# Performance work log

Hardware: AMD Instinct MI355X
Metric: run time of the kernel (lower is better)

The kernel has to match this reference:

```python
import jax, jax.numpy as jnp
import numpy as np

M, L, P, KK = 8, 3, 12, 9  # n_heads, n_levels, n_points, patch_size**2

def lrelu(v):
    return jnp.where(v >= 0, v, 0.1 * v)

def conv2d(x, w, b, pad):
    y = jax.lax.conv_general_dilated(x, w, (1, 1), [(pad, pad), (pad, pad)], dimension_numbers=('NCHW', 'OIHW', 'NCHW'))
    return y + b[None, :, None, None]

def trunk(x, w1, b1, w2, b2, w3, b3, w4, b4):
    h = lrelu(conv2d(x, w1, b1, 0))
    h = lrelu(conv2d(h, w2, b2, 1))
    h = lrelu(conv2d(h, w3, b3, 1))
    return conv2d(h, w4, b4, 0)

def grid_sample(img, gx, gy, align_corners):
    # img [N,C,H,W]; gx,gy [N,Q] normalized to [-1,1]; bilinear, zeros padding
    N, C, H, W = img.shape
    if align_corners:
        ix = (gx + 1.0) * 0.5 * (W - 1)
        iy = (gy + 1.0) * 0.5 * (H - 1)
    else:
        ix = ((gx + 1.0) * W - 1.0) * 0.5
        iy = ((gy + 1.0) * H - 1.0) * 0.5
    ix0 = jnp.floor(ix); iy0 = jnp.floor(iy)
    wx1 = ix - ix0; wy1 = iy - iy0
    flat = img.reshape(N, C, H * W)
    def gather(xi, yi, wgt):
        valid = (xi >= 0) & (xi <= W - 1) & (yi >= 0) & (yi <= H - 1)
        idx = (jnp.clip(yi, 0, H - 1) * W + jnp.clip(xi, 0, W - 1)).astype(jnp.int32)
        v = jnp.take_along_axis(flat, idx[:, None, :], axis=2)
        return v * (wgt * valid)[:, None, :]
    return (gather(ix0, iy0, (1 - wx1) * (1 - wy1)) + gather(ix0 + 1, iy0, wx1 * (1 - wy1))
            + gather(ix0, iy0 + 1, (1 - wx1) * wy1) + gather(ix0 + 1, iy0 + 1, wx1 * wy1))

def flow_warp(img, flow):
    # img [n,c,h,w]; flow [n,2,h,w] in pixels; torch grid_sample align_corners=True, zeros padding
    n, c, h, w = img.shape
    gy, gx = jnp.meshgrid(jnp.arange(h, dtype=img.dtype), jnp.arange(w, dtype=img.dtype), indexing='ij')
    gxn = 2.0 * (gx[None] + flow[:, 0]) / max(w - 1, 1) - 1.0
    gyn = 2.0 * (gy[None] + flow[:, 1]) / max(h - 1, 1) - 1.0
    return grid_sample(img, gxn.reshape(n, -1), gyn.reshape(n, -1), True).reshape(n, c, h, w)

def msdeform_attn(value, loc, attn, h, w):
    # pytorch MSDeformAttn core: value [N,L*HW,M,D]; loc [N,HW,M,L,Pt,2]; attn [N,HW,M,L,Pt]
    N, _, _, D = value.shape
    HW = h * w
    Pt = loc.shape[4]
    grids = 2.0 * loc - 1.0
    sampled = []
    for l in range(L):
        v = value[:, l * HW:(l + 1) * HW].transpose(0, 2, 3, 1).reshape(N * M, D, h, w)
        g = grids[:, :, :, l].transpose(0, 2, 1, 3, 4).reshape(N * M, HW * Pt, 2)
        s = grid_sample(v, g[..., 0], g[..., 1], False)  # [N*M, D, HW*Pt]
        sampled.append(s.reshape(N * M, D, HW, Pt))
    sampled = jnp.concatenate(sampled, axis=-1)  # [N*M, D, HW, L*Pt]
    aw = attn.transpose(0, 2, 1, 3, 4).reshape(N * M, HW, L * Pt)
    out = jnp.einsum('ndqp,nqp->nqd', sampled, aw)
    return out.reshape(N, M, HW, D).transpose(0, 2, 1, 3).reshape(N, HW, M * D)

def _forward(x, flow_1, flow_2, flip_flow_1, flip_flow_2, aw_w1, aw_b1, aw_w2, aw_b2, aw_w3, aw_b3, aw_w4, aw_b4, so_w1, so_b1, so_w2, so_b2, so_w3, so_b3, so_w4, so_b4, po_w1, po_b1, po_w2, po_b2, po_w3, po_b3, po_w4, po_b4, vp_w, vp_b, op_w1, op_b1, op_w2, op_b2):
    n, t, c, h, w = x.shape
    HW = h * w
    flow_cn1 = flow_1
    flow_cn2 = flow_1 + flow_warp(flow_2, flow_cn1)
    warp1 = flow_warp(x[:, 1], flow_cn1)
    warp2 = flow_warp(x[:, 2], flow_cn2)
    extra = jnp.concatenate([x[:, 0], warp1, warp2, flow_cn1, flow_cn2], axis=1)  # [n, 3c+4, h, w]
    value = conv2d(x.reshape(n, t * c, h, w), vp_w, vp_b, 0)
    off = trunk(extra, so_w1, so_b1, so_w2, so_b2, so_w3, so_b3, so_w4, so_b4)
    aw = trunk(extra, aw_w1, aw_b1, aw_w2, aw_b2, aw_w3, aw_b3, aw_w4, aw_b4)
    po = trunk(extra, po_w1, po_b1, po_w2, po_b2, po_w3, po_b3, po_w4, po_b4)
    value = value.reshape(n, t, c, HW).transpose(0, 1, 3, 2).reshape(n, t * HW, M, c // M)
    off = off.reshape(n, -1, HW).transpose(0, 2, 1).reshape(n, HW, M, L, P, 2)
    po = po.reshape(n, -1, HW).transpose(0, 2, 1).reshape(n, HW, M, L, P)
    po = jax.nn.sigmoid(po) * 3.0
    aw = aw.reshape(n, -1, HW).transpose(0, 2, 1).reshape(n, HW, M, L * P * KK)
    aw = jax.nn.softmax(aw, axis=-1).reshape(n, HW, M, L, P * KK)
    # flow-guided per-level offsets: level0 zeros, level1 flow_cn1, level2 flow_cn2
    f1 = flow_cn1.reshape(n, 2, HW).transpose(0, 2, 1)
    f2 = flow_cn2.reshape(n, 2, HW).transpose(0, 2, 1)
    fstack = jnp.stack([jnp.zeros_like(f1), f1, f2], axis=2)  # [n,HW,L,2]
    off = off + fstack[:, :, None, :, None, :]
    # 3x3 patch around each sampling point, scaled by learned patch offsets
    a = jnp.arange(-1, 2, dtype=x.dtype)
    pnx, pny = jnp.meshgrid(a, a, indexing='ij')
    p_n = jnp.stack([pnx, pny], axis=-1).reshape(KK, 2)
    off = off[..., None, :] + p_n * po[..., None, None]  # [n,HW,M,L,P,KK,2]
    off = off.reshape(n, HW, M, L, P * KK, 2)
    # reference points (valid ratios == 1)
    ry = (jnp.arange(h, dtype=x.dtype) + 0.5) / h
    rx = (jnp.arange(w, dtype=x.dtype) + 0.5) / w
    gy, gx = jnp.meshgrid(ry, rx, indexing='ij')
    ref = jnp.stack([gx, gy], axis=-1).reshape(1, HW, 1, 1, 1, 2)
    norm = jnp.array([w, h], dtype=x.dtype)
    loc = ref + off / norm
    out = msdeform_attn(value, loc, aw, h, w)  # [n, HW, c]
    feat = out.reshape(n, h, w, c).transpose(0, 3, 1, 2)
    res = conv2d(lrelu(conv2d(feat, op_w1, op_b1, 0)), op_w2, op_b2, 0)
    return res + x[:, 0]

def setup_inputs():
    key = jax.random.key(0)
    keys = jax.random.split(key, 64)
    it = iter(range(64))
    def nrm(shape, scale):
        return jax.random.normal(keys[next(it)], shape, jnp.float32) * scale
    n, t, c, h, w = 1, 3, 64, 64, 64
    Cin = t * c + 4  # 196
    d = {}
    d['x'] = nrm((n, t, c, h, w), 1.0)
    for nm in ['flow_1', 'flow_2', 'flip_flow_1', 'flip_flow_2']:
        d[nm] = nrm((n, 2, h, w), 1.5)
    def branch(prefix, out_ch, final_scale):
        d[prefix + '_w1'] = nrm((64, Cin, 1, 1), 1.0 / np.sqrt(Cin))
        d[prefix + '_b1'] = nrm((64,), 0.01)
        d[prefix + '_w2'] = nrm((64, 64, 3, 3), 1.0 / np.sqrt(64 * 9))
        d[prefix + '_b2'] = nrm((64,), 0.01)
        d[prefix + '_w3'] = nrm((64, 64, 3, 3), 1.0 / np.sqrt(64 * 9))
        d[prefix + '_b3'] = nrm((64,), 0.01)
        d[prefix + '_w4'] = nrm((out_ch, 64, 1, 1), final_scale)
        d[prefix + '_b4'] = nrm((out_ch,), 0.01)
    branch('aw', M * L * P * KK, 0.01)
    branch('so', M * L * P * 2, 0.01)
    branch('po', M * L * P, 0.01)
    d['vp_w'] = nrm((t * c, t * c, 1, 1), 1.0 / np.sqrt(t * c))
    d['vp_b'] = nrm((t * c,), 0.01)
    d['op_w1'] = nrm((c, c, 1, 1), 1.0 / np.sqrt(c))
    d['op_b1'] = nrm((c,), 0.01)
    d['op_w2'] = nrm((c, c, 1, 1), 1.0 / np.sqrt(c))
    d['op_b2'] = nrm((c,), 0.01)
    return d

def reference(x, flow_1, flow_2, flip_flow_1, flip_flow_2, aw_w1, aw_b1, aw_w2, aw_b2, aw_w3, aw_b3, aw_w4, aw_b4, so_w1, so_b1, so_w2, so_b2, so_w3, so_b3, so_w4, so_b4, po_w1, po_b1, po_w2, po_b2, po_w3, po_b3, po_w4, po_b4, vp_w, vp_b, op_w1, op_b1, op_w2, op_b2):
    return _forward(x, flow_1, flow_2, flip_flow_1, flip_flow_2, aw_w1, aw_b1, aw_w2, aw_b2, aw_w3, aw_b3, aw_w4, aw_b4, so_w1, so_b1, so_w2, so_b2, so_w3, so_b3, so_w4, so_b4, po_w1, po_b1, po_w2, po_b2, po_w3, po_b3, po_w4, po_b4, vp_w, vp_b, op_w1, op_b1, op_w2, op_b2)
```

## Files before the change

kernel.cpp:

```cpp
#include <hip/hip_runtime.h>
#include <hip/hip_bf16.h>
#include <math.h>

#define HWN 4096
#define VROW 72
#define VYP 36
#define VSZ_B (24 * VYP * VROW * 16)

typedef __attribute__((ext_vector_type(8))) short short8;
typedef __attribute__((ext_vector_type(4))) float f32x4;
typedef __attribute__((ext_vector_type(2))) float f32x2;

__device__ __forceinline__ float lrelu_f(float v) { return v >= 0.f ? v : 0.1f * v; }

__device__ __forceinline__ unsigned short f2bf(float f) {
  union { float f; unsigned u; } v; v.f = f;
  unsigned r = v.u + 0x7fff + ((v.u >> 16) & 1);
  return (unsigned short)(r >> 16);
}
__device__ __forceinline__ float bf2f(unsigned short u) {
  union { unsigned u; float f; } v; v.u = ((unsigned)u) << 16; return v.f;
}
__device__ __forceinline__ float bf_lo(unsigned u) {
  union { unsigned u; float f; } v; v.u = u << 16; return v.f;
}
__device__ __forceinline__ float bf_hi(unsigned u) {
  union { unsigned u; float f; } v; v.u = u & 0xffff0000u; return v.f;
}
template <bool HI>
__device__ __forceinline__ f32x2 cvt8(unsigned u) {
  return __builtin_amdgcn_cvt_pk_f32_fp8((int)u, HI);
}

__device__ __forceinline__ float bilin_zero(const float* __restrict__ img, float ix, float iy) {
  float fx0 = floorf(ix), fy0 = floorf(iy);
  int x0 = (int)fx0, y0 = (int)fy0;
  float wx1 = ix - fx0, wy1 = iy - fy0;
  float wx0 = 1.f - wx1, wy0 = 1.f - wy1;
  float acc = 0.f;
  if ((unsigned)y0 < 64u) {
    if ((unsigned)x0 < 64u)       acc += wx0 * wy0 * img[y0 * 64 + x0];
    if ((unsigned)(x0 + 1) < 64u) acc += wx1 * wy0 * img[y0 * 64 + x0 + 1];
  }
  if ((unsigned)(y0 + 1) < 64u) {
    if ((unsigned)x0 < 64u)       acc += wx0 * wy1 * img[(y0 + 1) * 64 + x0];
    if ((unsigned)(x0 + 1) < 64u) acc += wx1 * wy1 * img[(y0 + 1) * 64 + x0 + 1];
  }
  return acc;
}

__global__ void k_pre(
    const float* __restrict__ x, const float* __restrict__ flow1, const float* __restrict__ flow2,
    const float* so_w4, const float* po_w4, const float* aw_w4,
    const float* so_b4, const float* po_b4, const float* aw_b4,
    const float* so_b1, const float* po_b1, const float* aw_b1,
    const float* so_b2, const float* po_b2, const float* aw_b2,
    const float* so_b3, const float* po_b3, const float* aw_b3,
    const float* so_w1, const float* po_w1, const float* aw_w1,
    const float* so_w2, const float* po_w2, const float* aw_w2,
    const float* so_w3, const float* po_w3, const float* aw_w3,
    const float* op_w1, const float* op_w2, const float* vp_w,
    unsigned short* Wtail, float* btail, float* b1c, float* b2c, float* b3c,
    unsigned short* o1b, unsigned short* o2b, unsigned short* W1,
    unsigned short* W2g, unsigned short* W3g, unsigned short* vpb,
    unsigned short* xb, float* fcn2, unsigned char* v8) {
  __shared__ unsigned short tile[64 * 65];
  __shared__ unsigned short wrow[576];
  int gx = blockIdx.x;
  int tid = threadIdx.x;
  if (gx < 864) {
    int t = gx * 256 + tid;
    int row = t >> 6, k = t & 63;
    float v = row < 576 ? so_w4[row * 64 + k]
            : row < 864 ? po_w4[(row - 576) * 64 + k]
                        : aw_w4[(row - 864) * 64 + k];
    Wtail[t] = f2bf(v);
  } else if (gx < 912) {
    int t = (gx - 864) * 256 + tid;
    if (t < 3456) {
      btail[t] = t < 576 ? so_b4[t] : t < 864 ? po_b4[t - 576] : aw_b4[t - 864];
    } else if (t < 3648) {
      int i = t - 3456; b1c[i] = i < 64 ? so_b1[i] : i < 128 ? po_b1[i - 64] : aw_b1[i - 128];
    } else if (t < 3840) {
      int i = t - 3648; b2c[i] = i < 64 ? so_b2[i] : i < 128 ? po_b2[i - 64] : aw_b2[i - 128];
    } else if (t < 4032) {
      int i = t - 3840; b3c[i] = i < 64 ? so_b3[i] : i < 128 ? po_b3[i - 64] : aw_b3[i - 128];
    } else if (t < 8128) {
      o1b[t - 4032] = f2bf(op_w1[t - 4032]);
    } else if (t < 12224) {
      o2b[t - 8128] = f2bf(op_w2[t - 8128]);
    }
  } else if (gx < 1080) {
    int t = (gx - 912) * 256 + tid;
    if (t < 192 * 224) {
      int row = t / 224, k = t % 224;
      int tr = row >> 6, lco = row & 63;
      const float* s = tr == 0 ? so_w1 : tr == 1 ? po_w1 : aw_w1;
      W1[t] = (k < 196) ? f2bf(s[lco * 196 + k]) : (unsigned short)0;
    }
  } else if (gx < 1464) {
    int b = gx - 1080;
    int which = b >= 192;
    b &= 191;
    int tr = b >> 6, co = b & 63;
    const float* s;
    if (!which) s = tr == 0 ? so_w2 : tr == 1 ? po_w2 : aw_w2;
    else        s = tr == 0 ? so_w3 : tr == 1 ? po_w3 : aw_w3;
    unsigned short* d = which ? W3g : W2g;
#pragma unroll
    for (int j = tid; j < 576; j += 256) wrow[j] = f2bf(s[co * 576 + j]);
    __syncthreads();
#pragma unroll
    for (int j = tid; j < 576; j += 256)
      d[((size_t)tr * 64 + co) * 576 + j] = wrow[(j & 63) * 9 + (j >> 6)];
  } else if (gx < 1608) {
    int t = (gx - 1464) * 256 + tid;
    if (t < 192 * 192) vpb[t] = f2bf(vp_w[t]);
  } else if (gx < 1800) {
    int b = gx - 1608;
    int ptile = b & 63, cg = b >> 6;
    int px = tid & 63, ch0 = (tid >> 6) * 16;
#pragma unroll
    for (int i = 0; i < 16; i++) {
      float v = x[(size_t)(cg * 64 + ch0 + i) * HWN + ptile * 64 + px];
      tile[(ch0 + i) * 65 + px] = f2bf(v);
    }
    __syncthreads();
    int c = tid & 63, pl0 = (tid >> 6) * 16;
#pragma unroll
    for (int i = 0; i < 16; i++)
      xb[(size_t)(ptile * 64 + pl0 + i) * 192 + cg * 64 + c] = tile[c * 65 + pl0 + i];
  } else if (gx < 1816) {
    int p = (gx - 1800) * 256 + tid;
    int px = p & 63, py = p >> 6;
    float fx = flow1[p], fy = flow1[HWN + p];
    float ix = (float)px + fx, iy = (float)py + fy;
    fcn2[p] = fx + bilin_zero(flow2, ix, iy);
    fcn2[HWN + p] = fy + bilin_zero(flow2 + HWN, ix, iy);
  } else {
    int i = (gx - 1816) * 256 + tid;
    if (i < 2 * VSZ_B / 16) ((uint4*)v8)[i] = make_uint4(0, 0, 0, 0);
  }
}

__global__ void k_extra(const unsigned short* __restrict__ xb, const float* __restrict__ flow1,
                        const float* __restrict__ fcn2, unsigned short* __restrict__ extra) {
  int w = threadIdx.x >> 6, c = threadIdx.x & 63;
  int p = blockIdx.x * 4 + w;
  int px = p & 63, py = p >> 6;
  float fx1 = flow1[p], fy1 = flow1[HWN + p];
  float fx2 = fcn2[p],  fy2 = fcn2[HWN + p];
  extra[(size_t)p * 224 + c] = xb[(size_t)p * 192 + c];
#pragma unroll
  for (int lev = 0; lev < 2; lev++) {
    float ix = (float)px + (lev ? fx2 : fx1);
    float iy = (float)py + (lev ? fy2 : fy1);
    float fx0 = floorf(ix), fy0 = floorf(iy);
    int x0 = (int)fx0, y0 = (int)fy0;
    float wx1 = ix - fx0, wy1 = iy - fy0;
    float wx0 = 1.f - wx1, wy0 = 1.f - wy1;
    int coff = (lev + 1) * 64;
    float acc = 0.f;
    if ((unsigned)y0 < 64u) {
      if ((unsigned)x0 < 64u)       acc += wx0 * wy0 * bf2f(xb[(size_t)(y0 * 64 + x0) * 192 + coff + c]);
      if ((unsigned)(x0 + 1) < 64u) acc += wx1 * wy0 * bf2f(xb[(size_t)(y0 * 64 + x0 + 1) * 192 + coff + c]);
    }
    if ((unsigned)(y0 + 1) < 64u) {
      if ((unsigned)x0 < 64u)       acc += wx0 * wy1 * bf2f(xb[(size_t)((y0 + 1) * 64 + x0) * 192 + coff + c]);
      if ((unsigned)(x0 + 1) < 64u) acc += wx1 * wy1 * bf2f(xb[(size_t)((y0 + 1) * 64 + x0 + 1) * 192 + coff + c]);
    }
    extra[(size_t)p * 224 + coff + c] = f2bf(acc);
  }
  if (c < 2) {
    extra[(size_t)p * 224 + 192 + c] = f2bf(flow1[c * HWN + p]);
    extra[(size_t)p * 224 + 194 + c] = f2bf(fcn2[c * HWN + p]);
  }
  if (c < 28) extra[(size_t)p * 224 + 196 + c] = 0;
}

__global__ __launch_bounds__(128) void k_gemm2(
    const unsigned short* __restrict__ A0, const unsigned short* __restrict__ Wm0,
    const float* __restrict__ bias0, unsigned short* __restrict__ out0,
    const unsigned short* __restrict__ A1, const unsigned short* __restrict__ Wm1,
    const float* __restrict__ bias1, unsigned short* __restrict__ out1) {
  int z = blockIdx.z;
  const unsigned short* A = z ? A1 : A0;
  const unsigned short* Wm = z ? Wm1 : Wm0;
  const float* bias = z ? bias1 : bias0;
  unsigned short* out = z ? out1 : out0;
  int K = z ? 224 : 192;

  int wv = threadIdx.x >> 6;
  int l = threadIdx.x & 63;
  int lm = l & 15, lq = l >> 4;
  int p0 = blockIdx.x * 32 + wv * 16;
  int co0 = blockIdx.y * 32;

  f32x4 acc[2];
#pragma unroll
  for (int nt = 0; nt < 2; nt++) {
    float bv = bias[co0 + nt * 16 + lm];
    acc[nt] = (f32x4){bv, bv, bv, bv};
  }
  const unsigned short* ap = A + (size_t)(p0 + lm) * K + lq * 8;
  const unsigned short* wp = Wm + (size_t)(co0 + lm) * K + lq * 8;
  for (int k0 = 0; k0 < K; k0 += 32) {
    short8 af = *(const short8*)(ap + k0);
#pragma unroll
    for (int nt = 0; nt < 2; nt++) {
      short8 bf = *(const short8*)(wp + (size_t)nt * 16 * K + k0);
      acc[nt] = __builtin_amdgcn_mfma_f32_16x16x32_bf16(af, bf, acc[nt], 0, 0, 0);
    }
  }
#pragma unroll
  for (int nt = 0; nt < 2; nt++) {
    int co = co0 + nt * 16 + lm;
#pragma unroll
    for (int r = 0; r < 4; r++) {
      int p = p0 + lq * 4 + r;
      float v = acc[nt][r];
      if (z) v = lrelu_f(v);
      out[(size_t)p * 192 + co] = f2bf(v);
    }
  }
}

__global__ __launch_bounds__(128) void k_conv3g(const unsigned short* __restrict__ h,
                                                const unsigned short* __restrict__ Wm,
                                                const float* __restrict__ bias,
                                                unsigned short* __restrict__ out) {
  int wv = threadIdx.x >> 6;
  int l = threadIdx.x & 63;
  int lm = l & 15, lq = l >> 4;
  int p0 = blockIdx.x * 32 + wv * 16;
  int co0 = blockIdx.y * 16;
  int t = blockIdx.z;
  int p = p0 + lm;
  int px = p & 63, py = p >> 6;

  float bv = bias[t * 64 + co0 + lm];
  f32x4 acc = (f32x4){bv, bv, bv, bv};
  const unsigned short* wp = Wm + ((size_t)t * 64 + co0 + lm) * 576 + lq * 8;
#pragma unroll
  for (int kidx = 0; kidx < 9; kidx++) {
    int ky = kidx / 3, kx = kidx % 3;
    int pp = p + (ky - 1) * 64 + (kx - 1);
    bool valid = ((unsigned)(px + kx - 1) < 64u) && ((unsigned)(py + ky - 1) < 64u);
    const unsigned short* apb = h + (size_t)pp * 192 + t * 64 + lq * 8;
#pragma unroll
    for (int c2 = 0; c2 < 2; c2++) {
      short8 af = {};
      if (valid) af = *(const short8*)(apb + c2 * 32);
      short8 bf = *(const short8*)(wp + kidx * 64 + c2 * 32);
      acc = __builtin_amdgcn_mfma_f32_16x16x32_bf16(af, bf, acc, 0, 0, 0);
    }
  }
#pragma unroll
  for (int r = 0; r < 4; r++) {
    int po_ = p0 + lq * 4 + r;
    out[(size_t)po_ * 192 + t * 64 + co0 + lm] = f2bf(lrelu_f(acc[r]));
  }
}

__global__ __launch_bounds__(256) void k_tail(const unsigned short* __restrict__ A,
                                              const unsigned short* __restrict__ Wm,
                                              const float* __restrict__ bias,
                                              unsigned short* __restrict__ out,
                                              const unsigned short* __restrict__ vsb,
                                              unsigned char* __restrict__ v8) {
  if (blockIdx.y >= 108) {
    int i = ((blockIdx.y - 108) * 64 + blockIdx.x) * 256 + threadIdx.x;
    int lm = i % 24, p = i / 24;
    uint4 vv = ((const uint4*)vsb)[p * 24 + lm];
    int lo = 0, hi = 0;
    lo = __builtin_amdgcn_cvt_pk_fp8_f32(bf_lo(vv.x), bf_hi(vv.x), lo, false);
    lo = __builtin_amdgcn_cvt_pk_fp8_f32(bf_lo(vv.y), bf_hi(vv.y), lo, true);
    hi = __builtin_amdgcn_cvt_pk_fp8_f32(bf_lo(vv.z), bf_hi(vv.z), hi, false);
    hi = __builtin_amdgcn_cvt_pk_fp8_f32(bf_lo(vv.w), bf_hi(vv.w), hi, true);
    uint2 pk; pk.x = (unsigned)lo; pk.y = (unsigned)hi;
    int y = p >> 6, xx = p & 63;
    int ypA = (y >> 1) + 1, slotA = y & 1;
    int ypB = (y + 1) >> 1, slotB = (y & 1) ^ 1;
    *(uint2*)(v8 + (((lm * VYP + ypA) * VROW + xx + 2) * 16 + slotA * 8)) = pk;
    *(uint2*)(v8 + VSZ_B + (((lm * VYP + ypB) * VROW + xx + 2) * 16 + slotB * 8)) = pk;
    return;
  }
  int wv = threadIdx.x >> 6;
  int l = threadIdx.x & 63;
  int lm = l & 15, lq = l >> 4;
  int p0 = blockIdx.x * 64 + wv * 16;
  int co0 = blockIdx.y * 32;
  int t = (co0 < 576) ? 0 : (co0 < 864 ? 1 : 2);

  f32x4 acc[2];
#pragma unroll
  for (int nt = 0; nt < 2; nt++) {
    float bv = bias[co0 + nt * 16 + lm];
    acc[nt] = (f32x4){bv, bv, bv, bv};
  }
  const unsigned short* ap = A + (size_t)(p0 + lm) * 192 + t * 64 + lq * 8;
  const unsigned short* wp = Wm + (size_t)(co0 + lm) * 64 + lq * 8;
#pragma unroll
  for (int k0 = 0; k0 < 64; k0 += 32) {
    short8 af = *(const short8*)(ap + k0);
#pragma unroll
    for (int nt = 0; nt < 2; nt++) {
      short8 bf = *(const short8*)(wp + (size_t)nt * 16 * 64 + k0);
      acc[nt] = __builtin_amdgcn_mfma_f32_16x16x32_bf16(af, bf, acc[nt], 0, 0, 0);
    }
  }
#pragma unroll
  for (int nt = 0; nt < 2; nt++) {
    int co = co0 + nt * 16 + lm;
#pragma unroll
    for (int r = 0; r < 4; r++) {
      int p = p0 + lq * 4 + r;
      float v = acc[nt][r];
      if (t == 2) v = __expf(v);
      else if (t == 1) v = 3.f * __builtin_amdgcn_rcpf(1.f + __expf(-v));
      out[(size_t)p * 3456 + co] = f2bf(v);
    }
  }
}

__global__ __launch_bounds__(256, 4) void k_msdeform(
    const unsigned char* __restrict__ v8,
    const unsigned short* __restrict__ to,
    const float* __restrict__ flow1, const float* __restrict__ fcn2,
    unsigned short* __restrict__ featb) {
  int yl = threadIdx.x & 15;
  int p = blockIdx.x * 16 + (threadIdx.x >> 4);
  int m = blockIdx.y;
  int px = p & 63, py = p >> 6;

  float fx1 = flow1[p], fy1 = flow1[HWN + p];
  float fx2 = fcn2[p],  fy2 = fcn2[HWN + p];

  const unsigned short* row = to + (size_t)p * 3456;

  f32x2 accv[4];
#pragma unroll
  for (int d = 0; d < 4; d++) accv[d] = (f32x2){0.f, 0.f};
  float wsum = 0.f;

#pragma unroll 1
  for (int pair = yl; pair < 36; pair += 16) {
    int lv = pair / 12, pt = pair % 12;
    float fx = (lv == 1) ? fx1 : ((lv == 2) ? fx2 : 0.f);
    float fy = (lv == 1) ? fy1 : ((lv == 2) ? fy2 : 0.f);
    int ch = (m * 3 + lv) * 12 + pt;
    unsigned ow = *(const unsigned*)(row + ch * 2);
    float ox = bf_lo(ow);
    float oy = bf_hi(ow);
    float s = bf2f(row[576 + ch]);
    float bx = (float)px + ox + fx;
    float by = (float)py + oy + fy;
    int lmoff = (lv * 8 + m) * (VYP * VROW * 16);
    const unsigned short* lgp = row + 864 + m * 324 + lv * 108 + pt * 9;
#pragma unroll 3
    for (int kk = 0; kk < 9; kk++) {
      float pnx = (float)(kk / 3 - 1);
      float pny = (float)(kk % 3 - 1);
      float ix = bx + pnx * s;
      float iy = by + pny * s;
      float wgt = bf2f(lgp[kk]);
      wsum += wgt;

      float fx0 = floorf(ix), fy0 = floorf(iy);
      float wx1 = ix - fx0, wy1 = iy - fy0;
      float wx0 = 1.f - wx1, wy0 = 1.f - wy1;
      int x0 = min(max((int)fx0, -2), 66);
      int y0 = min(max((int)fy0, -2), 66);
      int par = y0 & 1;
      int yp = (y0 + 2 - par) >> 1;
      const unsigned char* vb = v8 + par * VSZ_B + lmoff + (yp * VROW + x0 + 2) * 16;

      uint4 qa = *(const uint4*)vb;
      uint4 qb = *(const uint4*)(vb + 16);

      float w00 = wgt * wx0 * wy0, w01 = wgt * wx0 * wy1;
      float w10 = wgt * wx1 * wy0, w11 = wgt * wx1 * wy1;
      f32x2 W00 = (f32x2){w00, w00}, W01 = (f32x2){w01, w01};
      f32x2 W10 = (f32x2){w10, w10}, W11 = (f32x2){w11, w11};

      accv[0] += W00 * cvt8<false>(qa.x) + W01 * cvt8<false>(qa.z)
               + W10 * cvt8<false>(qb.x) + W11 * cvt8<false>(qb.z);
      accv[1] += W00 * cvt8<true>(qa.x)  + W01 * cvt8<true>(qa.z)
               + W10 * cvt8<true>(qb.x)  + W11 * cvt8<true>(qb.z);
      accv[2] += W00 * cvt8<false>(qa.y) + W01 * cvt8<false>(qa.w)
               + W10 * cvt8<false>(qb.y) + W11 * cvt8<false>(qb.w);
      accv[3] += W00 * cvt8<true>(qa.y)  + W01 * cvt8<true>(qa.w)
               + W10 * cvt8<true>(qb.y)  + W11 * cvt8<true>(qb.w);
    }
  }
#pragma unroll
  for (int mask = 1; mask < 16; mask <<= 1) {
    wsum += __shfl_xor(wsum, mask);
#pragma unroll
    for (int d = 0; d < 4; d++) {
      accv[d].x += __shfl_xor(accv[d].x, mask);
      accv[d].y += __shfl_xor(accv[d].y, mask);
    }
  }
  if (yl < 8) {
    float inv = __builtin_amdgcn_rcpf(wsum);
    float r = 0.f;
#pragma unroll
    for (int d = 0; d < 8; d++) {
      float v = (d & 1) ? accv[d >> 1].y : accv[d >> 1].x;
      r = (d == yl) ? v : r;
    }
    featb[(size_t)p * 64 + m * 8 + yl] = f2bf(r * inv);
  }
}

__global__ __launch_bounds__(128) void k_opout(const unsigned short* __restrict__ featb,
                                               const unsigned short* __restrict__ o1b,
                                               const float* __restrict__ bias1,
                                               const unsigned short* __restrict__ o2b,
                                               const float* __restrict__ bias2,
                                               const float* __restrict__ x,
                                               float* __restrict__ out) {
  __shared__ unsigned short hop[32 * 72];
  int wv = threadIdx.x >> 6;
  int l = threadIdx.x & 63;
  int lm = l & 15, lq = l >> 4;
  int bp0 = blockIdx.x * 32;

  f32x4 acc1[4];
#pragma unroll
  for (int nt = 0; nt < 4; nt++) {
    float bv = bias1[nt * 16 + lm];
    acc1[nt] = (f32x4){bv, bv, bv, bv};
  }
  const unsigned short* ap = featb + (size_t)(bp0 + wv * 16 + lm) * 64 + lq * 8;
#pragma unroll
  for (int k0 = 0; k0 < 64; k0 += 32) {
    short8 af = *(const short8*)(ap + k0);
#pragma unroll
    for (int nt = 0; nt < 4; nt++) {
      short8 bf = *(const short8*)(o1b + (size_t)(nt * 16 + lm) * 64 + lq * 8 + k0);
      acc1[nt] = __builtin_amdgcn_mfma_f32_16x16x32_bf16(af, bf, acc1[nt], 0, 0, 0);
    }
  }
#pragma unroll
  for (int nt = 0; nt < 4; nt++)
#pragma unroll
    for (int r = 0; r < 4; r++)
      hop[(wv * 16 + lq * 4 + r) * 72 + nt * 16 + lm] = f2bf(lrelu_f(acc1[nt][r]));
  __syncthreads();

#pragma unroll
  for (int ct = 0; ct < 2; ct++) {
    int co0 = (wv * 2 + ct) * 16;
    f32x4 b4;
#pragma unroll
    for (int r = 0; r < 4; r++) b4[r] = bias2[co0 + lq * 4 + r];
#pragma unroll
    for (int pg = 0; pg < 2; pg++) {
      f32x4 a2 = b4;
#pragma unroll
      for (int k0 = 0; k0 < 64; k0 += 32) {
        short8 af = *(const short8*)(o2b + (size_t)(co0 + lm) * 64 + k0 + lq * 8);
        short8 bf = *(const short8*)(hop + (pg * 16 + lm) * 72 + k0 + lq * 8);
        a2 = __builtin_amdgcn_mfma_f32_16x16x32_bf16(af, bf, a2, 0, 0, 0);
      }
#pragma unroll
      for (int r = 0; r < 4; r++) {
        int co = co0 + lq * 4 + r;
        int p = bp0 + pg * 16 + lm;
        out[(size_t)co * HWN + p] = a2[r] + x[(size_t)co * HWN + p];
      }
    }
  }
}

extern "C" void kernel_launch(void* const* d_in, const int* in_sizes, int n_in,
                              void* d_out, int out_size, void* d_ws, size_t ws_size,
                              hipStream_t stream) {
  const float* x     = (const float*)d_in[0];
  const float* flow1 = (const float*)d_in[1];
  const float* flow2 = (const float*)d_in[2];
  const float* aw_w1 = (const float*)d_in[5];
  const float* aw_b1 = (const float*)d_in[6];
  const float* aw_w2 = (const float*)d_in[7];
  const float* aw_b2 = (const float*)d_in[8];
  const float* aw_w3 = (const float*)d_in[9];
  const float* aw_b3 = (const float*)d_in[10];
  const float* aw_w4 = (const float*)d_in[11];
  const float* aw_b4 = (const float*)d_in[12];
  const float* so_w1 = (const float*)d_in[13];
  const float* so_b1 = (const float*)d_in[14];
  const float* so_w2 = (const float*)d_in[15];
  const float* so_b2 = (const float*)d_in[16];
  const float* so_w3 = (const float*)d_in[17];
  const float* so_b3 = (const float*)d_in[18];
  const float* so_w4 = (const float*)d_in[19];
  const float* so_b4 = (const float*)d_in[20];
  const float* po_w1 = (const float*)d_in[21];
  const float* po_b1 = (const float*)d_in[22];
  const float* po_w2 = (const float*)d_in[23];
  const float* po_b2 = (const float*)d_in[24];
  const float* po_w3 = (const float*)d_in[25];
  const float* po_b3 = (const float*)d_in[26];
  const float* po_w4 = (const float*)d_in[27];
  const float* po_b4 = (const float*)d_in[28];
  const float* vp_w  = (const float*)d_in[29];
  const float* vp_b  = (const float*)d_in[30];
  const float* op_w1 = (const float*)d_in[31];
  const float* op_b1 = (const float*)d_in[32];
  const float* op_w2 = (const float*)d_in[33];
  const float* op_b2 = (const float*)d_in[34];

  char* base = (char*)d_ws;
  size_t off = 0;
  auto alloc = [&](size_t bytes) { void* pp = base + off; off = (off + bytes + 255) & ~(size_t)255; return pp; };

  float* fcn2  = (float*)alloc(2 * HWN * 4);
  unsigned short* xb    = (unsigned short*)alloc(192 * HWN * 2);
  unsigned short* vsb   = (unsigned short*)alloc(192 * HWN * 2);
  unsigned short* extra = (unsigned short*)alloc(224 * HWN * 2);
  unsigned short* h1    = (unsigned short*)alloc(192 * HWN * 2);
  unsigned short* h2    = (unsigned short*)alloc(192 * HWN * 2);
  unsigned short* h3    = (unsigned short*)alloc(192 * HWN * 2);
  unsigned short* to    = (unsigned short*)alloc((size_t)3456 * HWN * 2);
  unsigned short* featb = (unsigned short*)alloc(64 * HWN * 2);
  unsigned char* v8     = (unsigned char*)alloc((size_t)VSZ_B * 2);
  unsigned short* Wtail = (unsigned short*)alloc(3456 * 64 * 2);
  float* btail = (float*)alloc(3456 * 4);
  float* b1c   = (float*)alloc(192 * 4);
  float* b2c   = (float*)alloc(192 * 4);
  float* b3c   = (float*)alloc(192 * 4);
  unsigned short* o1b = (unsigned short*)alloc(64 * 64 * 2);
  unsigned short* o2b = (unsigned short*)alloc(64 * 64 * 2);
  unsigned short* W1  = (unsigned short*)alloc(192 * 224 * 2);
  unsigned short* W2g = (unsigned short*)alloc(3 * 64 * 576 * 2);
  unsigned short* W3g = (unsigned short*)alloc(3 * 64 * 576 * 2);
  unsigned short* vpb = (unsigned short*)alloc(192 * 192 * 2);

  k_pre<<<2302, 256, 0, stream>>>(
      x, flow1, flow2,
      so_w4, po_w4, aw_w4, so_b4, po_b4, aw_b4,
      so_b1, po_b1, aw_b1, so_b2, po_b2, aw_b2, so_b3, po_b3, aw_b3,
      so_w1, po_w1, aw_w1, so_w2, po_w2, aw_w2, so_w3, po_w3, aw_w3,
      op_w1, op_w2, vp_w,
      Wtail, btail, b1c, b2c, b3c, o1b, o2b, W1, W2g, W3g, vpb, xb, fcn2, v8);

  k_extra<<<1024, 256, 0, stream>>>(xb, flow1, fcn2, extra);

  k_gemm2<<<dim3(128, 6, 2), 128, 0, stream>>>(xb, vpb, vp_b, vsb, extra, W1, b1c, h1);

  k_conv3g<<<dim3(128, 4, 3), 128, 0, stream>>>(h1, W2g, b2c, h2);
  k_conv3g<<<dim3(128, 4, 3), 128, 0, stream>>>(h2, W3g, b3c, h3);
  k_tail<<<dim3(64, 114), 256, 0, stream>>>(h3, Wtail, btail, to, vsb, v8);

  k_msdeform<<<dim3(256, 8), 256, 0, stream>>>(v8, to, flow1, fcn2, featb);

  k_opout<<<128, 128, 0, stream>>>(featb, o1b, op_b1, o2b, op_b2, x, (float*)d_out);
}
```

Baseline: 224.7 us.

## Fuse deformable sampling with output projection and hoist per-row bilinear setup

Merges the deformable-attention sampling kernel and the two-layer output projection into one kernel. Each block now handles 2 pixels across all 8 heads, and the features stay in shared memory in fp32 instead of taking a bf16 round trip through global memory. The 3x3 patch loop is split so the y-row address and y weights are computed once per row rather than per tap. The output MLP now uses scalar FMA dot products instead of MFMA, and writes to the output are strided by pixel, which risks uncoalesced stores and idle threads during the projection phase.

```diff
diff --git a/kernel.cpp b/kernel.cpp
--- a/kernel.cpp
+++ b/kernel.cpp
@@ -323,14 +323,20 @@
   }
 }
 
-__global__ __launch_bounds__(256, 4) void k_msdeform(
+__global__ __launch_bounds__(256, 4) void k_msdout(
     const unsigned char* __restrict__ v8,
     const unsigned short* __restrict__ to,
     const float* __restrict__ flow1, const float* __restrict__ fcn2,
-    unsigned short* __restrict__ featb) {
-  int yl = threadIdx.x & 15;
-  int p = blockIdx.x * 16 + (threadIdx.x >> 4);
-  int m = blockIdx.y;
+    const unsigned short* __restrict__ o1b, const float* __restrict__ bias1,
+    const unsigned short* __restrict__ o2b, const float* __restrict__ bias2,
+    const float* __restrict__ x, float* __restrict__ out) {
+  __shared__ float featL[2][64];
+  __shared__ float hopL[2][64];
+  int tid = threadIdx.x;
+  int yl = tid & 15;
+  int m = (tid >> 4) & 7;
+  int pl = tid >> 7;
+  int p = blockIdx.x * 2 + pl;
   int px = p & 63, py = p >> 6;
 
   float fx1 = flow1[p], fy1 = flow1[HWN + p];
@@ -357,40 +363,48 @@
     float by = (float)py + oy + fy;
     int lmoff = (lv * 8 + m) * (VYP * VROW * 16);
     const unsigned short* lgp = row + 864 + m * 324 + lv * 108 + pt * 9;
-#pragma unroll 3
-    for (int kk = 0; kk < 9; kk++) {
-      float pnx = (float)(kk / 3 - 1);
-      float pny = (float)(kk % 3 - 1);
-      float ix = bx + pnx * s;
-      float iy = by + pny * s;
-      float wgt = bf2f(lgp[kk]);
-      wsum += wgt;
-
-      float fx0 = floorf(ix), fy0 = floorf(iy);
-      float wx1 = ix - fx0, wy1 = iy - fy0;
-      float wx0 = 1.f - wx1, wy0 = 1.f - wy1;
-      int x0 = min(max((int)fx0, -2), 66);
+
+    const unsigned char* rb[3];
+    float yw0[3], yw1[3];
+#pragma unroll
+    for (int j = 0; j < 3; j++) {
+      float cy = by + (float)(j - 1) * s;
+      float fy0 = floorf(cy);
+      yw1[j] = cy - fy0; yw0[j] = 1.f - yw1[j];
       int y0 = min(max((int)fy0, -2), 66);
       int par = y0 & 1;
       int yp = (y0 + 2 - par) >> 1;
-      const unsigned char* vb = v8 + par * VSZ_B + lmoff + (yp * VROW + x0 + 2) * 16;
-
-      uint4 qa = *(const uint4*)vb;
-      uint4 qb = *(const uint4*)(vb + 16);
-
-      float w00 = wgt * wx0 * wy0, w01 = wgt * wx0 * wy1;
-      float w10 = wgt * wx1 * wy0, w11 = wgt * wx1 * wy1;
-      f32x2 W00 = (f32x2){w00, w00}, W01 = (f32x2){w01, w01};
-      f32x2 W10 = (f32x2){w10, w10}, W11 = (f32x2){w11, w11};
-
-      accv[0] += W00 * cvt8<false>(qa.x) + W01 * cvt8<false>(qa.z)
-               + W10 * cvt8<false>(qb.x) + W11 * cvt8<false>(qb.z);
-      accv[1] += W00 * cvt8<true>(qa.x)  + W01 * cvt8<true>(qa.z)
-               + W10 * cvt8<true>(qb.x)  + W11 * cvt8<true>(qb.z);
-      accv[2] += W00 * cvt8<false>(qa.y) + W01 * cvt8<false>(qa.w)
-               + W10 * cvt8<false>(qb.y) + W11 * cvt8<false>(qb.w);
-      accv[3] += W00 * cvt8<true>(qa.y)  + W01 * cvt8<true>(qa.w)
-               + W10 * cvt8<true>(qb.y)  + W11 * cvt8<true>(qb.w);
+      rb[j] = v8 + par * VSZ_B + lmoff + yp * (VROW * 16);
+    }
+#pragma unroll 1
+    for (int jx = 0; jx < 3; jx++) {
+      float cx = bx + (float)(jx - 1) * s;
+      float fx0 = floorf(cx);
+      float wx1 = cx - fx0, wx0 = 1.f - wx1;
+      int xoff = (min(max((int)fx0, -2), 66) + 2) * 16;
+      const unsigned short* lg3 = lgp + jx * 3;
+#pragma unroll
+      for (int jy = 0; jy < 3; jy++) {
+        float wgt = bf2f(lg3[jy]);
+        wsum += wgt;
+        const unsigned char* vb = rb[jy] + xoff;
+        uint4 qa = *(const uint4*)vb;
+        uint4 qb = *(const uint4*)(vb + 16);
+
+        float w00 = wgt * wx0 * yw0[jy], w01 = wgt * wx0 * yw1[jy];
+        float w10 = wgt * wx1 * yw0[jy], w11 = wgt * wx1 * yw1[jy];
+        f32x2 W00 = (f32x2){w00, w00}, W01 = (f32x2){w01, w01};
+        f32x2 W10 = (f32x2){w10, w10}, W11 = (f32x2){w11, w11};
+
+        accv[0] += W00 * cvt8<false>(qa.x) + W01 * cvt8<false>(qa.z)
+                 + W10 * cvt8<false>(qb.x) + W11 * cvt8<false>(qb.z);
+        accv[1] += W00 * cvt8<true>(qa.x)  + W01 * cvt8<true>(qa.z)
+                 + W10 * cvt8<true>(qb.x)  + W11 * cvt8<true>(qb.z);
+        accv[2] += W00 * cvt8<false>(qa.y) + W01 * cvt8<false>(qa.w)
+                 + W10 * cvt8<false>(qb.y) + W11 * cvt8<false>(qb.w);
+        accv[3] += W00 * cvt8<true>(qa.y)  + W01 * cvt8<true>(qa.w)
+                 + W10 * cvt8<true>(qb.y)  + W11 * cvt8<true>(qb.w);
+      }
     }
   }
 #pragma unroll
@@ -410,68 +424,42 @@
       float v = (d & 1) ? accv[d >> 1].y : accv[d >> 1].x;
       r = (d == yl) ? v : r;
     }
-    featb[(size_t)p * 64 + m * 8 + yl] = f2bf(r * inv);
-  }
-}
-
-__global__ __launch_bounds__(128) void k_opout(const unsigned short* __restrict__ featb,
-                                               const unsigned short* __restrict__ o1b,
-                                               const float* __restrict__ bias1,
-                                               const unsigned short* __restrict__ o2b,
-                                               const float* __restrict__ bias2,
-                                               const float* __restrict__ x,
-                                               float* __restrict__ out) {
-  __shared__ unsigned short hop[32 * 72];
-  int wv = threadIdx.x >> 6;
-  int l = threadIdx.x & 63;
-  int lm = l & 15, lq = l >> 4;
-  int bp0 = blockIdx.x * 32;
-
-  f32x4 acc1[4];
-#pragma unroll
-  for (int nt = 0; nt < 4; nt++) {
-    float bv = bias1[nt * 16 + lm];
-    acc1[nt] = (f32x4){bv, bv, bv, bv};
-  }
-  const unsigned short* ap = featb + (size_t)(bp0 + wv * 16 + lm) * 64 + lq * 8;
-#pragma unroll
-  for (int k0 = 0; k0 < 64; k0 += 32) {
-    short8 af = *(const short8*)(ap + k0);
-#pragma unroll
-    for (int nt = 0; nt < 4; nt++) {
-      short8 bf = *(const short8*)(o1b + (size_t)(nt * 16 + lm) * 64 + lq * 8 + k0);
-      acc1[nt] = __builtin_amdgcn_mfma_f32_16x16x32_bf16(af, bf, acc1[nt], 0, 0, 0);
-    }
-  }
-#pragma unroll
-  for (int nt = 0; nt < 4; nt++)
-#pragma unroll
-    for (int r = 0; r < 4; r++)
-      hop[(wv * 16 + lq * 4 + r) * 72 + nt * 16 + lm] = f2bf(lrelu_f(acc1[nt][r]));
+    featL[pl][m * 8 + yl] = r * inv;
+  }
   __syncthreads();
 
-#pragma unroll
-  for (int ct = 0; ct < 2; ct++) {
-    int co0 = (wv * 2 + ct) * 16;
-    f32x4 b4;
-#pragma unroll
-    for (int r = 0; r < 4; r++) b4[r] = bias2[co0 + lq * 4 + r];
-#pragma unroll
-    for (int pg = 0; pg < 2; pg++) {
-      f32x4 a2 = b4;
-#pragma unroll
-      for (int k0 = 0; k0 < 64; k0 += 32) {
-        short8 af = *(const short8*)(o2b + (size_t)(co0 + lm) * 64 + k0 + lq * 8);
-        short8 bf = *(const short8*)(hop + (pg * 16 + lm) * 72 + k0 + lq * 8);
-        a2 = __builtin_amdgcn_mfma_f32_16x16x32_bf16(af, bf, a2, 0, 0, 0);
-      }
-#pragma unroll
-      for (int r = 0; r < 4; r++) {
-        int co = co0 + lq * 4 + r;
-        int p = bp0 + pg * 16 + lm;
-        out[(size_t)co * HWN + p] = a2[r] + x[(size_t)co * HWN + p];
-      }
-    }
+  if (tid < 128) {
+    int ql = tid >> 6, co = tid & 63;
+    float a = bias1[co];
+    const uint4* wr = (const uint4*)(o1b + co * 64);
+#pragma unroll
+    for (int c8 = 0; c8 < 8; c8++) {
+      uint4 wv = wr[c8];
+      int ci = c8 * 8;
+      a += bf_lo(wv.x) * featL[ql][ci]     + bf_hi(wv.x) * featL[ql][ci + 1]
+         + bf_lo(wv.y) * featL[ql][ci + 2] + bf_hi(wv.y) * featL[ql][ci + 3]
+         + bf_lo(wv.z) * featL[ql][ci + 4] + bf_hi(wv.z) * featL[ql][ci + 5]
+         + bf_lo(wv.w) * featL[ql][ci + 6] + bf_hi(wv.w) * featL[ql][ci + 7];
+    }
+    hopL[ql][co] = lrelu_f(a);
+  }
+  __syncthreads();
+
+  if (tid < 128) {
+    int ql = tid >> 6, co = tid & 63;
+    int p2 = blockIdx.x * 2 + ql;
+    float a = bias2[co];
+    const uint4* wr = (const uint4*)(o2b + co * 64);
+#pragma unroll
+    for (int c8 = 0; c8 < 8; c8++) {
+      uint4 wv = wr[c8];
+      int ci = c8 * 8;
+      a += bf_lo(wv.x) * hopL[ql][ci]     + bf_hi(wv.x) * hopL[ql][ci + 1]
+         + bf_lo(wv.y) * hopL[ql][ci + 2] + bf_hi(wv.y) * hopL[ql][ci + 3]
+         + bf_lo(wv.z) * hopL[ql][ci + 4] + bf_hi(wv.z) * hopL[ql][ci + 5]
+         + bf_lo(wv.w) * hopL[ql][ci + 6] + bf_hi(wv.w) * hopL[ql][ci + 7];
+    }
+    out[(size_t)co * HWN + p2] = a + x[(size_t)co * HWN + p2];
   }
 }
 
@@ -524,7 +512,6 @@
   unsigned short* h2    = (unsigned short*)alloc(192 * HWN * 2);
   unsigned short* h3    = (unsigned short*)alloc(192 * HWN * 2);
   unsigned short* to    = (unsigned short*)alloc((size_t)3456 * HWN * 2);
-  unsigned short* featb = (unsigned short*)alloc(64 * HWN * 2);
   unsigned char* v8     = (unsigned char*)alloc((size_t)VSZ_B * 2);
   unsigned short* Wtail = (unsigned short*)alloc(3456 * 64 * 2);
   float* btail = (float*)alloc(3456 * 4);
@@ -554,7 +541,5 @@
   k_conv3g<<<dim3(128, 4, 3), 128, 0, stream>>>(h2, W3g, b3c, h3);
   k_tail<<<dim3(64, 114), 256, 0, stream>>>(h3, Wtail, btail, to, vsb, v8);
 
-  k_msdeform<<<dim3(256, 8), 256, 0, stream>>>(v8, to, flow1, fcn2, featb);
-
-  k_opout<<<128, 128, 0, stream>>>(featb, o1b, op_b1, o2b, op_b2, x, (float*)d_out);
-}
+  k_msdout<<<2048, 256, 0, stream>>>(v8, to, flow1, fcn2, o1b, op_b1, o2b, op_b2, x, (float*)d_out);
+}
```

Measured after the change: 222.4 us (median of 2 runs). No clear change (-1.0%).
